# Kernel tuning notes

Hardware: AMD Instinct MI355X
Metric: run time of the kernel (lower is better)

Reference implementation:

```python
import jax, jax.numpy as jnp
import numpy as np

N_NODES = 50000


def _sage_conv(x, src, dst, Wl, bl, Wr):
    # mean aggregation of source-node features into target nodes
    agg = jax.ops.segment_sum(x[src], dst, num_segments=N_NODES)      # [N, C]
    deg = jax.ops.segment_sum(jnp.ones_like(src, dtype=x.dtype), dst,
                              num_segments=N_NODES)                   # [N]
    mean = agg / jnp.maximum(deg, 1.0)[:, None]
    # PyG SAGEConv: lin_l(aggr) (with bias) + lin_r(x) (no bias)
    return mean @ Wl.T + bl + x @ Wr.T


def setup_inputs() -> dict:
    key = jax.random.key(0)
    ks = jax.random.split(key, 8)
    C = 128
    E = 600000
    scale = 1.0 / np.sqrt(C)
    x = jax.random.normal(ks[0], (N_NODES, C), dtype=jnp.float32)
    edge_index = jax.random.randint(ks[1], (2, E), 0, N_NODES, dtype=jnp.int64)
    Wl1 = jax.random.normal(ks[2], (C, C), dtype=jnp.float32) * scale
    bl1 = jnp.zeros((C,), dtype=jnp.float32)
    Wr1 = jax.random.normal(ks[3], (C, C), dtype=jnp.float32) * scale
    Wl2 = jax.random.normal(ks[4], (C, C), dtype=jnp.float32) * scale
    bl2 = jnp.zeros((C,), dtype=jnp.float32)
    Wr2 = jax.random.normal(ks[5], (C, C), dtype=jnp.float32) * scale
    return {"x": x, "edge_index": edge_index, "Wl1": Wl1, "bl1": bl1,
            "Wr1": Wr1, "Wl2": Wl2, "bl2": bl2, "Wr2": Wr2}


def reference(x, edge_index, Wl1, bl1, Wr1, Wl2, bl2, Wr2):
    src, dst = edge_index[0], edge_index[1]
    h = _sage_conv(x, src, dst, Wl1, bl1, Wr1)
    h = jax.nn.relu(h)
    out = _sage_conv(h, src, dst, Wl2, bl2, Wr2)
    return out
```

## Files before the change

kernel.cpp:

```cpp
#include <hip/hip_runtime.h>
#include <hip/hip_bf16.h>

#define N_NODES 50000
#define C 128
#define NPAD 50176
#define NTILES (NPAD / 16)
#define GEMM_BLOCKS (NTILES / 8)
#define XPREP_BLOCKS 3125
#define WPREP_BLOCKS 256
#define CAP 48
#define CSTRIDE 32

typedef short bf16x8 __attribute__((ext_vector_type(8)));
typedef float f32x4 __attribute__((ext_vector_type(4)));

__device__ __forceinline__ unsigned short f2bf(float f) {
    unsigned int u = __float_as_uint(f);
    unsigned int r = u + 0x7fffu + ((u >> 16) & 1u);
    return (unsigned short)(r >> 16);
}

__device__ __forceinline__ float bf2f(unsigned short b) {
    return __uint_as_float(((unsigned int)b) << 16);
}

__device__ __forceinline__ void acc8(float* a, uint4 u) {
    const unsigned int uu[4] = {u.x, u.y, u.z, u.w};
#pragma unroll
    for (int i = 0; i < 4; ++i) {
        a[2 * i] += bf2f((unsigned short)uu[i]);
        a[2 * i + 1] += bf2f((unsigned short)(uu[i] >> 16));
    }
}

__global__ __launch_bounds__(256) void buildfill_kernel(
    const int* __restrict__ src, const int* __restrict__ dst, int E, int edgeBlocks,
    int* __restrict__ cursor, int* __restrict__ csr,
    const float* __restrict__ x, unsigned short* __restrict__ Xb,
    const float* __restrict__ Wl1, const float* __restrict__ Wr1,
    const float* __restrict__ Wl2, const float* __restrict__ Wr2,
    unsigned short* __restrict__ Wc1, unsigned short* __restrict__ Wc2) {
    int b = blockIdx.x;
    if (b < edgeBlocks) {
        int e = b * 256 + threadIdx.x;
        if (e < E) {
            int d = dst[e];
            int s = src[e];
            if ((unsigned)d < (unsigned)N_NODES && (unsigned)s < (unsigned)N_NODES) {
                int slot = atomicAdd(cursor + d * CSTRIDE, 1);
                if (slot < CAP) csr[d * CAP + slot] = s;
            }
        }
    } else if (b < edgeBlocks + XPREP_BLOCKS) {
        int t = (b - edgeBlocks) * 256 + threadIdx.x;
        if (t >= N_NODES * C / 8) return;
        const float4 a = *(const float4*)(x + (size_t)t * 8);
        const float4 c = *(const float4*)(x + (size_t)t * 8 + 4);
        unsigned short o[8] = {f2bf(a.x), f2bf(a.y), f2bf(a.z), f2bf(a.w),
                               f2bf(c.x), f2bf(c.y), f2bf(c.z), f2bf(c.w)};
        *(uint4*)(Xb + (size_t)t * 8) = *(const uint4*)o;
    } else {
        int idx = (b - edgeBlocks - XPREP_BLOCKS) * 256 + threadIdx.x;
        int layer = idx >> 15;
        int r = idx & 32767;
        int j = r >> 8, k = r & 255;
        const float* Wl = layer ? Wl2 : Wl1;
        const float* Wr = layer ? Wr2 : Wr1;
        unsigned short* Wc = layer ? Wc2 : Wc1;
        float f = (k < 128) ? Wl[j * 128 + k] : Wr[j * 128 + (k - 128)];
        Wc[r] = f2bf(f);
    }
}

__global__ __launch_bounds__(256) void gather_kernel(
    const unsigned short* __restrict__ feat,
    const int* __restrict__ cursor, const int* __restrict__ csr,
    unsigned short* __restrict__ Fm) {
    int w = (blockIdx.x * 256 + threadIdx.x) >> 6;
    int lane = threadIdx.x & 63;
    if (w >= N_NODES) return;
    const int g = lane >> 4;
    const int c = lane & 15;
    const int degraw = cursor[(size_t)w * CSTRIDE];
    const int myidx = (lane < CAP) ? csr[w * CAP + lane] : 0;
    const int deg = min(degraw, CAP);
    float a[8];
#pragma unroll
    for (int i = 0; i < 8; ++i) a[i] = 0.f;
    const unsigned short* fp = feat + c * 8;
    const int nb = (deg + 3) >> 2;
    uint4 u[6];
#pragma unroll
    for (int b = 0; b < 6; ++b) {
        if (b < nb) {
            int r = 4 * b + g;
            int s = __shfl(myidx, r < deg ? r : 0);
            u[b] = *(const uint4*)(fp + (size_t)s * C);
        }
    }
#pragma unroll
    for (int b = 0; b < 6; ++b) {
        if (b < nb) {
            if (4 * b + g < deg) acc8(a, u[b]);
        }
    }
    if (nb > 6) {
        for (int b = 6; b < nb; ++b) {
            int r = 4 * b + g;
            int s = __shfl(myidx, r < deg ? r : 0);
            uint4 uu = *(const uint4*)(fp + (size_t)s * C);
            if (r < deg) acc8(a, uu);
        }
    }
#pragma unroll
    for (int i = 0; i < 8; ++i) {
        a[i] += __shfl_xor(a[i], 16);
        a[i] += __shfl_xor(a[i], 32);
    }
    const float inv = 1.0f / fmaxf((float)deg, 1.0f);
    if (g == 0) {
        unsigned int o[4];
#pragma unroll
        for (int i = 0; i < 4; ++i)
            o[i] = (unsigned)f2bf(a[2 * i] * inv) |
                   ((unsigned)f2bf(a[2 * i + 1] * inv) << 16);
        *(uint4*)(Fm + (size_t)w * C + c * 8) = *(const uint4*)o;
    }
}

__global__ __launch_bounds__(256) void sage_gemm(
    const unsigned short* __restrict__ Fm,
    const unsigned short* __restrict__ Self,
    const unsigned short* __restrict__ Wc,
    const float* __restrict__ bias,
    void* __restrict__ outv, int relu, int obf16) {
    __shared__ unsigned short wl[128 * 264];
    for (int cidx = threadIdx.x; cidx < 4096; cidx += 256) {
        int row = cidx >> 5, chunk = cidx & 31;
        const uint4 v = *(const uint4*)(Wc + row * 256 + chunk * 8);
        *(uint4*)(&wl[row * 264 + chunk * 8]) = v;
    }
    __syncthreads();

    const int wave = threadIdx.x >> 6;
    const int lane = threadIdx.x & 63;
    const int m = lane & 15;
    const int q = lane >> 4;
    const int tile0 = blockIdx.x * 8 + wave * 2;

    const size_t rowoff = (size_t)(tile0 * 16 + m) * C + q * 8;
    const unsigned short* am = Fm + rowoff;
    const unsigned short* as = Self + rowoff;

    f32x4 acc[2][8];
#pragma unroll
    for (int t = 0; t < 2; ++t)
#pragma unroll
        for (int j = 0; j < 8; ++j) acc[t][j] = (f32x4){0.f, 0.f, 0.f, 0.f};

#pragma unroll
    for (int kt = 0; kt < 8; ++kt) {
        const unsigned short* A = (kt < 4) ? am : as;
        const int ko = (kt & 3) * 32;
        bf16x8 af0 = *(const bf16x8*)(A + ko);
        bf16x8 af1 = *(const bf16x8*)(A + 16 * C + ko);
#pragma unroll
        for (int jt = 0; jt < 8; ++jt) {
            bf16x8 bfrag = *(const bf16x8*)(&wl[(jt * 16 + m) * 264 + kt * 32 + q * 8]);
            acc[0][jt] = __builtin_amdgcn_mfma_f32_16x16x32_bf16(af0, bfrag, acc[0][jt], 0, 0, 0);
            acc[1][jt] = __builtin_amdgcn_mfma_f32_16x16x32_bf16(af1, bfrag, acc[1][jt], 0, 0, 0);
        }
    }

#pragma unroll
    for (int t = 0; t < 2; ++t) {
        int rbase = (tile0 + t) * 16 + q * 4;
#pragma unroll
        for (int r = 0; r < 4; ++r) {
            int row = rbase + r;
            if (row < N_NODES) {
#pragma unroll
                for (int jt = 0; jt < 8; ++jt) {
                    int col = jt * 16 + m;
                    float v = acc[t][jt][r] + bias[col];
                    if (relu) v = fmaxf(v, 0.0f);
                    if (obf16)
                        ((unsigned short*)outv)[(size_t)row * C + col] = f2bf(v);
                    else
                        ((float*)outv)[(size_t)row * C + col] = v;
                }
            }
        }
    }
}

extern "C" void kernel_launch(void* const* d_in, const int* in_sizes, int n_in,
                              void* d_out, int out_size, void* d_ws, size_t ws_size,
                              hipStream_t stream) {
    const float* x = (const float*)d_in[0];
    const int* edge = (const int*)d_in[1];
    const float* Wl1 = (const float*)d_in[2];
    const float* bl1 = (const float*)d_in[3];
    const float* Wr1 = (const float*)d_in[4];
    const float* Wl2 = (const float*)d_in[5];
    const float* bl2 = (const float*)d_in[6];
    const float* Wr2 = (const float*)d_in[7];
    float* out = (float*)d_out;

    const int E = in_sizes[1] / 2;
    const int* src = edge;
    const int* dst = edge + E;

    char* ws = (char*)d_ws;
    size_t off = 0;
    int* cursor = (int*)(ws + off);           off += (size_t)N_NODES * CSTRIDE * 4;
    off = (off + 511) & ~511ull;
    int* csr = (int*)(ws + off);              off += (size_t)N_NODES * CAP * 4;
    off = (off + 511) & ~511ull;
    unsigned short* Xb = (unsigned short*)(ws + off); off += (size_t)NPAD * C * 2;
    unsigned short* Fm = (unsigned short*)(ws + off); off += (size_t)NPAD * C * 2;
    unsigned short* h  = (unsigned short*)(ws + off); off += (size_t)NPAD * C * 2;
    unsigned short* Wc1 = (unsigned short*)(ws + off); off += 128 * 256 * 2;
    unsigned short* Wc2 = (unsigned short*)(ws + off); off += 128 * 256 * 2;
    (void)ws_size;

    const int edgeBlocks = (E + 255) / 256;
    const int gatherBlocks = (NPAD * 64) / 256;

    hipMemsetAsync(cursor, 0, (size_t)N_NODES * CSTRIDE * 4, stream);
    buildfill_kernel<<<edgeBlocks + XPREP_BLOCKS + WPREP_BLOCKS, 256, 0, stream>>>(
        src, dst, E, edgeBlocks, cursor, csr, x, Xb, Wl1, Wr1, Wl2, Wr2, Wc1, Wc2);

    gather_kernel<<<gatherBlocks, 256, 0, stream>>>(Xb, cursor, csr, Fm);
    sage_gemm<<<GEMM_BLOCKS, 256, 0, stream>>>(Fm, Xb, Wc1, bl1, h, 1, 1);

    gather_kernel<<<gatherBlocks, 256, 0, stream>>>(h, cursor, csr, Fm);
    sage_gemm<<<GEMM_BLOCKS, 256, 0, stream>>>(Fm, h, Wc2, bl2, out, 0, 0);
}
```

Baseline: 208.7 us.

## Fuse neighbor mean-gather with SAGE GEMM via shared-memory tile

```diff
diff --git a/kernel.cpp b/kernel.cpp
--- a/kernel.cpp
+++ b/kernel.cpp
@@ -4,12 +4,12 @@
 #define N_NODES 50000
 #define C 128
 #define NPAD 50176
-#define NTILES (NPAD / 16)
-#define GEMM_BLOCKS (NTILES / 8)
+#define FUSED_BLOCKS (NPAD / 64)
 #define XPREP_BLOCKS 3125
 #define WPREP_BLOCKS 256
 #define CAP 48
 #define CSTRIDE 32
+#define FPITCH 132
 
 typedef short bf16x8 __attribute__((ext_vector_type(8)));
 typedef float f32x4 __attribute__((ext_vector_type(4)));
@@ -72,123 +72,111 @@
     }
 }
 
-__global__ __launch_bounds__(256) void gather_kernel(
+__global__ __launch_bounds__(256, 4) void sage_fused(
     const unsigned short* __restrict__ feat,
     const int* __restrict__ cursor, const int* __restrict__ csr,
-    unsigned short* __restrict__ Fm) {
-    int w = (blockIdx.x * 256 + threadIdx.x) >> 6;
-    int lane = threadIdx.x & 63;
-    if (w >= N_NODES) return;
-    const int g = lane >> 4;
-    const int c = lane & 15;
-    const int degraw = cursor[(size_t)w * CSTRIDE];
-    const int myidx = (lane < CAP) ? csr[w * CAP + lane] : 0;
-    const int deg = min(degraw, CAP);
-    float a[8];
-#pragma unroll
-    for (int i = 0; i < 8; ++i) a[i] = 0.f;
-    const unsigned short* fp = feat + c * 8;
-    const int nb = (deg + 3) >> 2;
-    uint4 u[6];
-#pragma unroll
-    for (int b = 0; b < 6; ++b) {
-        if (b < nb) {
-            int r = 4 * b + g;
-            int s = __shfl(myidx, r < deg ? r : 0);
-            u[b] = *(const uint4*)(fp + (size_t)s * C);
-        }
-    }
-#pragma unroll
-    for (int b = 0; b < 6; ++b) {
-        if (b < nb) {
-            if (4 * b + g < deg) acc8(a, u[b]);
-        }
-    }
-    if (nb > 6) {
-        for (int b = 6; b < nb; ++b) {
-            int r = 4 * b + g;
-            int s = __shfl(myidx, r < deg ? r : 0);
-            uint4 uu = *(const uint4*)(fp + (size_t)s * C);
-            if (r < deg) acc8(a, uu);
-        }
-    }
-#pragma unroll
-    for (int i = 0; i < 8; ++i) {
-        a[i] += __shfl_xor(a[i], 16);
-        a[i] += __shfl_xor(a[i], 32);
-    }
-    const float inv = 1.0f / fmaxf((float)deg, 1.0f);
-    if (g == 0) {
-        unsigned int o[4];
-#pragma unroll
-        for (int i = 0; i < 4; ++i)
-            o[i] = (unsigned)f2bf(a[2 * i] * inv) |
-                   ((unsigned)f2bf(a[2 * i + 1] * inv) << 16);
-        *(uint4*)(Fm + (size_t)w * C + c * 8) = *(const uint4*)o;
-    }
-}
-
-__global__ __launch_bounds__(256) void sage_gemm(
-    const unsigned short* __restrict__ Fm,
-    const unsigned short* __restrict__ Self,
     const unsigned short* __restrict__ Wc,
     const float* __restrict__ bias,
     void* __restrict__ outv, int relu, int obf16) {
-    __shared__ unsigned short wl[128 * 264];
-    for (int cidx = threadIdx.x; cidx < 4096; cidx += 256) {
-        int row = cidx >> 5, chunk = cidx & 31;
-        const uint4 v = *(const uint4*)(Wc + row * 256 + chunk * 8);
-        *(uint4*)(&wl[row * 264 + chunk * 8]) = v;
+    __shared__ unsigned short fm[64 * FPITCH];
+
+    const int lane = threadIdx.x & 63;
+    const int w = threadIdx.x >> 6;
+    const int g = lane >> 4;
+    const int c = lane & 15;
+    const int base = blockIdx.x * 64;
+    const unsigned short* fp = feat + c * 8;
+
+#pragma unroll 1
+    for (int i = 0; i < 16; ++i) {
+        const int rl = w * 16 + i;
+        const int node = base + rl;
+        if (node < N_NODES) {
+            const int degraw = cursor[(size_t)node * CSTRIDE];
+            const int myidx = (lane < CAP) ? csr[node * CAP + lane] : 0;
+            const int deg = min(degraw, CAP);
+            float a[8];
+#pragma unroll
+            for (int k = 0; k < 8; ++k) a[k] = 0.f;
+            const int nb = (deg + 3) >> 2;
+            uint4 u[6];
+#pragma unroll
+            for (int b = 0; b < 6; ++b) {
+                if (b < nb) {
+                    int r = 4 * b + g;
+                    int s = __shfl(myidx, r < deg ? r : 0);
+                    u[b] = *(const uint4*)(fp + (size_t)s * C);
+                }
+            }
+#pragma unroll
+            for (int b = 0; b < 6; ++b) {
+                if (b < nb && 4 * b + g < deg) acc8(a, u[b]);
+            }
+            if (nb > 6) {
+                for (int b = 6; b < nb; ++b) {
+                    int r = 4 * b + g;
+                    int s = __shfl(myidx, r < deg ? r : 0);
+                    uint4 uu = *(const uint4*)(fp + (size_t)s * C);
+                    if (r < deg) acc8(a, uu);
+                }
+            }
+#pragma unroll
+            for (int k = 0; k < 8; ++k) {
+                a[k] += __shfl_xor(a[k], 16);
+                a[k] += __shfl_xor(a[k], 32);
+            }
+            const float inv = 1.0f / fmaxf((float)deg, 1.0f);
+            if (g == 0) {
+                unsigned int o[4];
+#pragma unroll
+                for (int k = 0; k < 4; ++k)
+                    o[k] = (unsigned)f2bf(a[2 * k] * inv) |
+                           ((unsigned)f2bf(a[2 * k + 1] * inv) << 16);
+                *(uint4*)(&fm[rl * FPITCH + c * 8]) = *(const uint4*)o;
+            }
+        } else if (g == 0) {
+            const uint4 z = {0u, 0u, 0u, 0u};
+            *(uint4*)(&fm[rl * FPITCH + c * 8]) = z;
+        }
     }
     __syncthreads();
 
-    const int wave = threadIdx.x >> 6;
-    const int lane = threadIdx.x & 63;
     const int m = lane & 15;
     const int q = lane >> 4;
-    const int tile0 = blockIdx.x * 8 + wave * 2;
-
-    const size_t rowoff = (size_t)(tile0 * 16 + m) * C + q * 8;
-    const unsigned short* am = Fm + rowoff;
-    const unsigned short* as = Self + rowoff;
-
-    f32x4 acc[2][8];
-#pragma unroll
-    for (int t = 0; t < 2; ++t)
-#pragma unroll
-        for (int j = 0; j < 8; ++j) acc[t][j] = (f32x4){0.f, 0.f, 0.f, 0.f};
+    const unsigned short* as = feat + (size_t)(base + w * 16 + m) * C + q * 8;
+
+    f32x4 acc[8];
+#pragma unroll
+    for (int j = 0; j < 8; ++j) acc[j] = (f32x4){0.f, 0.f, 0.f, 0.f};
 
 #pragma unroll
     for (int kt = 0; kt < 8; ++kt) {
-        const unsigned short* A = (kt < 4) ? am : as;
-        const int ko = (kt & 3) * 32;
-        bf16x8 af0 = *(const bf16x8*)(A + ko);
-        bf16x8 af1 = *(const bf16x8*)(A + 16 * C + ko);
+        bf16x8 af;
+        if (kt < 4)
+            af = *(const bf16x8*)(&fm[(w * 16 + m) * FPITCH + kt * 32 + q * 8]);
+        else
+            af = *(const bf16x8*)(as + (kt & 3) * 32);
 #pragma unroll
         for (int jt = 0; jt < 8; ++jt) {
-            bf16x8 bfrag = *(const bf16x8*)(&wl[(jt * 16 + m) * 264 + kt * 32 + q * 8]);
-            acc[0][jt] = __builtin_amdgcn_mfma_f32_16x16x32_bf16(af0, bfrag, acc[0][jt], 0, 0, 0);
-            acc[1][jt] = __builtin_amdgcn_mfma_f32_16x16x32_bf16(af1, bfrag, acc[1][jt], 0, 0, 0);
-        }
-    }
-
-#pragma unroll
-    for (int t = 0; t < 2; ++t) {
-        int rbase = (tile0 + t) * 16 + q * 4;
-#pragma unroll
-        for (int r = 0; r < 4; ++r) {
-            int row = rbase + r;
-            if (row < N_NODES) {
-#pragma unroll
-                for (int jt = 0; jt < 8; ++jt) {
-                    int col = jt * 16 + m;
-                    float v = acc[t][jt][r] + bias[col];
-                    if (relu) v = fmaxf(v, 0.0f);
-                    if (obf16)
-                        ((unsigned short*)outv)[(size_t)row * C + col] = f2bf(v);
-                    else
-                        ((float*)outv)[(size_t)row * C + col] = v;
-                }
+            bf16x8 bfrag = *(const bf16x8*)(Wc + (jt * 16 + m) * 256 + kt * 32 + q * 8);
+            acc[jt] = __builtin_amdgcn_mfma_f32_16x16x32_bf16(af, bfrag, acc[jt], 0, 0, 0);
+        }
+    }
+
+    const int rbase = base + w * 16 + q * 4;
+#pragma unroll
+    for (int r = 0; r < 4; ++r) {
+        int row = rbase + r;
+        if (row < N_NODES) {
+#pragma unroll
+            for (int jt = 0; jt < 8; ++jt) {
+                int col = jt * 16 + m;
+                float v = acc[jt][r] + bias[col];
+                if (relu) v = fmaxf(v, 0.0f);
+                if (obf16)
+                    ((unsigned short*)outv)[(size_t)row * C + col] = f2bf(v);
+                else
+                    ((float*)outv)[(size_t)row * C + col] = v;
             }
         }
     }
@@ -218,22 +206,18 @@
     int* csr = (int*)(ws + off);              off += (size_t)N_NODES * CAP * 4;
     off = (off + 511) & ~511ull;
     unsigned short* Xb = (unsigned short*)(ws + off); off += (size_t)NPAD * C * 2;
-    unsigned short* Fm = (unsigned short*)(ws + off); off += (size_t)NPAD * C * 2;
     unsigned short* h  = (unsigned short*)(ws + off); off += (size_t)NPAD * C * 2;
     unsigned short* Wc1 = (unsigned short*)(ws + off); off += 128 * 256 * 2;
     unsigned short* Wc2 = (unsigned short*)(ws + off); off += 128 * 256 * 2;
     (void)ws_size;
 
     const int edgeBlocks = (E + 255) / 256;
-    const int gatherBlocks = (NPAD * 64) / 256;
 
     hipMemsetAsync(cursor, 0, (size_t)N_NODES * CSTRIDE * 4, stream);
     buildfill_kernel<<<edgeBlocks + XPREP_BLOCKS + WPREP_BLOCKS, 256, 0, stream>>>(
         src, dst, E, edgeBlocks, cursor, csr, x, Xb, Wl1, Wr1, Wl2, Wr2, Wc1, Wc2);
 
-    gather_kernel<<<gatherBlocks, 256, 0, stream>>>(Xb, cursor, csr, Fm);
-    sage_gemm<<<GEMM_BLOCKS, 256, 0, stream>>>(Fm, Xb, Wc1, bl1, h, 1, 1);
-
-    gather_kernel<<<gatherBlocks, 256, 0, stream>>>(h, cursor, csr, Fm);
-    sage_gemm<<<GEMM_BLOCKS, 256, 0, stream>>>(Fm, h, Wc2, bl2, out, 0, 0);
-}
+    sage_fused<<<FUSED_BLOCKS, 256, 0, stream>>>(Xb, cursor, csr, Wc1, bl1, h, 1, 1);
+
+    sage_fused<<<FUSED_BLOCKS, 256, 0, stream>>>(h, cursor, csr, Wc2, bl2, out, 0, 0);
+}
```

After: 245.8 us. 17.8% more time.
